# Performance work log

Hardware: AMD Instinct MI355X
Metric: run time of the kernel (lower is better)

## Reference

```python
import jax, jax.numpy as jnp
import numpy as np

N_NODES = 50000
IN_C, HID_C, OUT_C = 128, 128, 64
N_EDGES = 600000
DROPOUT_P = 0.5


def setup_inputs() -> dict:
    key = jax.random.key(0)
    k1, k2, k3, k4, k5, k6 = jax.random.split(key, 6)
    x = jax.random.normal(k1, (N_NODES, IN_C), dtype=jnp.float32)
    edge_index = jax.random.randint(k2, (2, N_EDGES), 0, N_NODES, dtype=jnp.int64)
    s1 = 1.0 / np.sqrt(IN_C)
    s2 = 1.0 / np.sqrt(HID_C)
    W1 = jax.random.uniform(k3, (IN_C, HID_C), jnp.float32, -s1, s1)
    b1 = jnp.zeros((HID_C,), jnp.float32)
    W2 = jax.random.uniform(k4, (HID_C, OUT_C), jnp.float32, -s2, s2)
    b2 = jnp.zeros((OUT_C,), jnp.float32)
    return {"x": x, "W1": W1, "b1": b1, "W2": W2, "b2": b2, "edge_index": edge_index}


def reference(x, W1, b1, W2, b2, edge_index):
    N = x.shape[0]
    self_loops = jnp.arange(N, dtype=edge_index.dtype)
    src = jnp.concatenate([edge_index[0], self_loops])  # [E+N]
    dst = jnp.concatenate([edge_index[1], self_loops])
    # symmetric GCN normalization with self-loops (gcn_norm)
    deg = jax.ops.segment_sum(jnp.ones(dst.shape, x.dtype), dst, num_segments=N)
    dinv = jnp.where(deg > 0, jax.lax.rsqrt(deg), 0.0)
    norm = dinv[src] * dinv[dst]  # [E+N]

    def conv(h, W, b):
        h = h @ W  # dense transform first (smaller message dim)
        msg = h[src] * norm[:, None]  # gather + scale, [E+N, C]
        return jax.ops.segment_sum(msg, dst, num_segments=N) + b

    h = jax.nn.relu(conv(x, W1, b1))
    # dropout p=0.5 with fixed key (training mode, deterministic reference)
    keep = jax.random.bernoulli(jax.random.key(42), 1.0 - DROPOUT_P, h.shape)
    h = jnp.where(keep, h / (1.0 - DROPOUT_P), 0.0)
    return conv(h, W2, b2)
```

## Files before the change

kernel.cpp:

```cpp
#include <hip/hip_runtime.h>


#define NN      50000
#define INC     128
#define HIDC    128
#define OUTC    64
#define NE      600000
#define NB      ((NN + 255) / 256)
#define CAP     64

typedef unsigned short bf16_t;
typedef short bf16x8 __attribute__((ext_vector_type(8)));
typedef float f32x4  __attribute__((ext_vector_type(4)));

__device__ __forceinline__ unsigned short f2bf(float f) {
  unsigned u = __float_as_uint(f);
  u += 0x7fffu + ((u >> 16) & 1u);
  return (unsigned short)(u >> 16);
}

__device__ __forceinline__ float dinv_of(int c) {
  return 1.0f / sqrtf((float)(c + 1));
}

__device__ __forceinline__ void tf_round(unsigned &x0, unsigned &x1, int r) {
  x0 += x1;
  x1 = (x1 << r) | (x1 >> (32 - r));
  x1 ^= x0;
}

__device__ __forceinline__ void threefry_0_42(unsigned &x0, unsigned &x1) {
  const unsigned ks0 = 0u, ks1 = 42u, ks2 = 0x1BD11BDAu ^ 42u;
  x0 += ks0; x1 += ks1;
  tf_round(x0,x1,13); tf_round(x0,x1,15); tf_round(x0,x1,26); tf_round(x0,x1, 6);
  x0 += ks1; x1 += ks2 + 1u;
  tf_round(x0,x1,17); tf_round(x0,x1,29); tf_round(x0,x1,16); tf_round(x0,x1,24);
  x0 += ks2; x1 += ks0 + 2u;
  tf_round(x0,x1,13); tf_round(x0,x1,15); tf_round(x0,x1,26); tf_round(x0,x1, 6);
  x0 += ks0; x1 += ks1 + 3u;
  tf_round(x0,x1,17); tf_round(x0,x1,29); tf_round(x0,x1,16); tf_round(x0,x1,24);
  x0 += ks1; x1 += ks2 + 4u;
  tf_round(x0,x1,13); tf_round(x0,x1,15); tf_round(x0,x1,26); tf_round(x0,x1, 6);
  x0 += ks2; x1 += ks0 + 5u;
}

__device__ __forceinline__ bool keep_bit(unsigned idx) {
  unsigned x0 = 0u, x1 = idx;
  threefry_0_42(x0, x1);
  return ((x0 ^ x1) & 0x80000000u) == 0u;
}

__global__ __launch_bounds__(256)
void prep0(const unsigned* __restrict__ ew, int* __restrict__ flag,
           int* __restrict__ cnt) {
  const int b = blockIdx.x, t = threadIdx.x;
  if (b < NB) {
    int idx = b * 256 + t;
    if (idx < NN) cnt[idx] = 0;
  } else {
    __shared__ unsigned acc[256];
    unsigned v = 0;
    for (int i = t; i < 2048; i += 256) v |= ew[2 * i + 1];
    acc[t] = v;
    __syncthreads();
    for (int s = 128; s > 0; s >>= 1) {
      if (t < s) acc[t] |= acc[t + s];
      __syncthreads();
    }
    if (t == 0) *flag = (acc[0] == 0u) ? 1 : 0;
  }
}

__global__ __launch_bounds__(256, 3)
void gemm1_bucket(const float* __restrict__ X, const float* __restrict__ W,
                  const void* __restrict__ ei, const int* __restrict__ flag,
                  int* __restrict__ cnt, int* __restrict__ ssrc,
                  bf16_t* __restrict__ Ab) {
  constexpr int C  = HIDC;
  constexpr int K  = 128;
  constexpr int KS = 136;
  constexpr int CT16 = C / 16;
  __shared__ bf16_t xs[64 * KS];
  __shared__ bf16_t wsT[C * KS];

  const int tid = threadIdx.x;
  const int rb  = blockIdx.x * 64;

  const int eb = blockIdx.x * 768;
  int es[3], ed[3];
  bool ev[3];
  const bool i64 = (*flag != 0);
#pragma unroll
  for (int j = 0; j < 3; j++) {
    int e = eb + j * 256 + tid;
    ev[j] = (e < NE);
    es[j] = 0; ed[j] = 0;
    if (ev[j]) {
      if (i64) {
        es[j] = (int)((const long long*)ei)[e];
        ed[j] = (int)((const long long*)ei)[NE + e];
      } else {
        es[j] = ((const int*)ei)[e];
        ed[j] = ((const int*)ei)[NE + e];
      }
    }
  }
  int slot[3];
#pragma unroll
  for (int j = 0; j < 3; j++)
    slot[j] = ev[j] ? atomicAdd(&cnt[ed[j]], 1) : CAP;

  for (int i = tid; i < C * (K / 8); i += 256) {
    int nn = i % C, kc = i / C;
    ushort4 lo, hi;
    lo.x = f2bf(W[(size_t)(kc * 8 + 0) * C + nn]);
    lo.y = f2bf(W[(size_t)(kc * 8 + 1) * C + nn]);
    lo.z = f2bf(W[(size_t)(kc * 8 + 2) * C + nn]);
    lo.w = f2bf(W[(size_t)(kc * 8 + 3) * C + nn]);
    hi.x = f2bf(W[(size_t)(kc * 8 + 4) * C + nn]);
    hi.y = f2bf(W[(size_t)(kc * 8 + 5) * C + nn]);
    hi.z = f2bf(W[(size_t)(kc * 8 + 6) * C + nn]);
    hi.w = f2bf(W[(size_t)(kc * 8 + 7) * C + nn]);
    *(ushort4*)&wsT[nn * KS + kc * 8]     = lo;
    *(ushort4*)&wsT[nn * KS + kc * 8 + 4] = hi;
  }
  for (int i = tid; i < 64 * (K / 4); i += 256) {
    int r = i >> 5, kq = i & 31;
    int row = rb + r;
    ushort4 o = make_ushort4(0, 0, 0, 0);
    if (row < NN) {
      float4 v = *(const float4*)(X + (size_t)row * K + kq * 4);
      o.x = f2bf(v.x); o.y = f2bf(v.y); o.z = f2bf(v.z); o.w = f2bf(v.w);
    }
    *(ushort4*)&xs[r * KS + kq * 4] = o;
  }

#pragma unroll
  for (int j = 0; j < 3; j++)
    if (ev[j] && slot[j] < CAP) ssrc[ed[j] * CAP + slot[j]] = es[j];

  __syncthreads();

  const int wv   = tid >> 6;
  const int lane = tid & 63;
  const int m    = lane & 15;
  const int q    = lane >> 4;

  f32x4 acc[CT16];
#pragma unroll
  for (int c = 0; c < CT16; c++) acc[c] = (f32x4){0.f, 0.f, 0.f, 0.f};

#pragma unroll
  for (int k0 = 0; k0 < K; k0 += 32) {
    bf16x8 a = *(bf16x8*)&xs[(wv * 16 + m) * KS + k0 + q * 8];
#pragma unroll
    for (int c = 0; c < CT16; c++) {
      bf16x8 b = *(bf16x8*)&wsT[(c * 16 + m) * KS + k0 + q * 8];
      acc[c] = __builtin_amdgcn_mfma_f32_16x16x32_bf16(a, b, acc[c], 0, 0, 0);
    }
  }

  const int rowq = rb + wv * 16 + q * 4;
#pragma unroll
  for (int r = 0; r < 4; r++) {
    int row = rowq + r;
    if (row < NN) {
#pragma unroll
      for (int c = 0; c < CT16; c++)
        Ab[(size_t)row * C + c * 16 + m] = f2bf(acc[c][r]);
    }
  }
}

template<int C, bool IN_BF16>
__global__ __launch_bounds__(256, 3)
void gemm_mfma(const void* __restrict__ Xv, const float* __restrict__ W,
               const int* __restrict__ cnt, bf16_t* __restrict__ Ab, int n) {
  constexpr int K  = 128;
  constexpr int KS = 136;
  constexpr int CT16 = C / 16;
  __shared__ bf16_t xs[64 * KS];
  __shared__ bf16_t wsT[C * KS];

  const int tid = threadIdx.x;
  const int rb  = blockIdx.x * 64;

  for (int i = tid; i < C * (K / 8); i += 256) {
    int nn = i % C, kc = i / C;
    ushort4 lo, hi;
    lo.x = f2bf(W[(size_t)(kc * 8 + 0) * C + nn]);
    lo.y = f2bf(W[(size_t)(kc * 8 + 1) * C + nn]);
    lo.z = f2bf(W[(size_t)(kc * 8 + 2) * C + nn]);
    lo.w = f2bf(W[(size_t)(kc * 8 + 3) * C + nn]);
    hi.x = f2bf(W[(size_t)(kc * 8 + 4) * C + nn]);
    hi.y = f2bf(W[(size_t)(kc * 8 + 5) * C + nn]);
    hi.z = f2bf(W[(size_t)(kc * 8 + 6) * C + nn]);
    hi.w = f2bf(W[(size_t)(kc * 8 + 7) * C + nn]);
    *(ushort4*)&wsT[nn * KS + kc * 8]     = lo;
    *(ushort4*)&wsT[nn * KS + kc * 8 + 4] = hi;
  }
  for (int i = tid; i < 64 * (K / 4); i += 256) {
    int r = i >> 5, kq = i & 31;
    int row = rb + r;
    ushort4 o = make_ushort4(0, 0, 0, 0);
    if (row < n) {
      if (IN_BF16) {
        o = *(const ushort4*)((const bf16_t*)Xv + (size_t)row * K + kq * 4);
      } else {
        float4 v = *(const float4*)((const float*)Xv + (size_t)row * K + kq * 4);
        o.x = f2bf(v.x); o.y = f2bf(v.y); o.z = f2bf(v.z); o.w = f2bf(v.w);
      }
    }
    *(ushort4*)&xs[r * KS + kq * 4] = o;
  }
  __syncthreads();

  const int wv   = tid >> 6;
  const int lane = tid & 63;
  const int m    = lane & 15;
  const int q    = lane >> 4;

  f32x4 acc[CT16];
#pragma unroll
  for (int c = 0; c < CT16; c++) acc[c] = (f32x4){0.f, 0.f, 0.f, 0.f};

#pragma unroll
  for (int k0 = 0; k0 < K; k0 += 32) {
    bf16x8 a = *(bf16x8*)&xs[(wv * 16 + m) * KS + k0 + q * 8];
#pragma unroll
    for (int c = 0; c < CT16; c++) {
      bf16x8 b = *(bf16x8*)&wsT[(c * 16 + m) * KS + k0 + q * 8];
      acc[c] = __builtin_amdgcn_mfma_f32_16x16x32_bf16(a, b, acc[c], 0, 0, 0);
    }
  }

  const int rowq = rb + wv * 16 + q * 4;
#pragma unroll
  for (int r = 0; r < 4; r++) {
    int row = rowq + r;
    if (row < n) {
      float dv = dinv_of(cnt[row]);
#pragma unroll
      for (int c = 0; c < CT16; c++)
        Ab[(size_t)row * C + c * 16 + m] = f2bf(acc[c][r] * dv);
    }
  }
}

__device__ __forceinline__ void acc_u2(float4 &a, uint2 v) {
  a.x += __uint_as_float(v.x << 16);
  a.y += __uint_as_float(v.x & 0xffff0000u);
  a.z += __uint_as_float(v.y << 16);
  a.w += __uint_as_float(v.y & 0xffff0000u);
}

__device__ __forceinline__ void acc_u2s(float4 &a, uint2 v, float dv) {
  a.x = fmaf(dv, __uint_as_float(v.x << 16),         a.x);
  a.y = fmaf(dv, __uint_as_float(v.x & 0xffff0000u), a.y);
  a.z = fmaf(dv, __uint_as_float(v.y << 16),         a.z);
  a.w = fmaf(dv, __uint_as_float(v.y & 0xffff0000u), a.w);
}

__device__ __forceinline__ float dinv_fast(int c) {
  return rsqrtf((float)(c + 1));
}

__global__ __launch_bounds__(256)
void agg1(const bf16_t* __restrict__ A1b, const int* __restrict__ cnt,
          const int* __restrict__ ssrc, const float* __restrict__ b1,
          bf16_t* __restrict__ Hb) {
  int node = (blockIdx.x * 256 + threadIdx.x) >> 5;
  int lane = threadIdx.x & 31;
  if (node >= NN) return;

  const uint2* A4 = (const uint2*)A1b;
  const int cn = cnt[node];
  const float dn = dinv_of(cn);
  float4 acc = make_float4(0.f, 0.f, 0.f, 0.f);
  acc_u2s(acc, A4[(size_t)node * 32 + lane], dn);
  int e = node * CAP;
  int end = e + min(cn, CAP);
  for (; e + 3 < end; e += 4) {
    int s0 = ssrc[e], s1 = ssrc[e+1], s2 = ssrc[e+2], s3 = ssrc[e+3];
    uint2 v0 = A4[(size_t)s0 * 32 + lane];
    uint2 v1 = A4[(size_t)s1 * 32 + lane];
    uint2 v2 = A4[(size_t)s2 * 32 + lane];
    uint2 v3 = A4[(size_t)s3 * 32 + lane];
    float q0 = dinv_fast(cnt[s0]);
    float q1 = dinv_fast(cnt[s1]);
    float q2 = dinv_fast(cnt[s2]);
    float q3 = dinv_fast(cnt[s3]);
    acc_u2s(acc, v0, q0); acc_u2s(acc, v1, q1);
    acc_u2s(acc, v2, q2); acc_u2s(acc, v3, q3);
  }
  for (; e < end; e++) {
    int s = ssrc[e];
    acc_u2s(acc, A4[(size_t)s * 32 + lane], dinv_fast(cnt[s]));
  }

  int col = lane * 4;
  float4 bb = *(const float4*)&b1[col];
  float h0 = fmaxf(acc.x * dn + bb.x, 0.f);
  float h1 = fmaxf(acc.y * dn + bb.y, 0.f);
  float h2 = fmaxf(acc.z * dn + bb.z, 0.f);
  float h3 = fmaxf(acc.w * dn + bb.w, 0.f);
  unsigned base = (unsigned)node * HIDC + (unsigned)col;
  ushort4 o;
  o.x = keep_bit(base)     ? f2bf(2.f * h0) : 0;
  o.y = keep_bit(base + 1) ? f2bf(2.f * h1) : 0;
  o.z = keep_bit(base + 2) ? f2bf(2.f * h2) : 0;
  o.w = keep_bit(base + 3) ? f2bf(2.f * h3) : 0;
  ((ushort4*)Hb)[(size_t)node * 32 + lane] = o;
}

__global__ __launch_bounds__(256)
void agg2(const bf16_t* __restrict__ A2b, const int* __restrict__ cnt,
          const int* __restrict__ ssrc, const float* __restrict__ b2,
          float* __restrict__ out) {
  int node = (blockIdx.x * 256 + threadIdx.x) >> 4;
  int lane = threadIdx.x & 15;
  if (node >= NN) return;

  const uint2* A4 = (const uint2*)A2b;
  const int cn = cnt[node];
  const float dn = dinv_of(cn);
  float4 acc = make_float4(0.f, 0.f, 0.f, 0.f);
  acc_u2(acc, A4[(size_t)node * 16 + lane]);
  int e = node * CAP;
  int end = e + min(cn, CAP);
  for (; e + 3 < end; e += 4) {
    int s0 = ssrc[e], s1 = ssrc[e+1], s2 = ssrc[e+2], s3 = ssrc[e+3];
    uint2 v0 = A4[(size_t)s0 * 16 + lane];
    uint2 v1 = A4[(size_t)s1 * 16 + lane];
    uint2 v2 = A4[(size_t)s2 * 16 + lane];
    uint2 v3 = A4[(size_t)s3 * 16 + lane];
    acc_u2(acc, v0); acc_u2(acc, v1); acc_u2(acc, v2); acc_u2(acc, v3);
  }
  for (; e < end; e++)
    acc_u2(acc, A4[(size_t)ssrc[e] * 16 + lane]);

  float4 bb = *(const float4*)&b2[lane * 4];
  ((float4*)out)[(size_t)node * 16 + lane] =
    make_float4(acc.x*dn + bb.x, acc.y*dn + bb.y, acc.z*dn + bb.z, acc.w*dn + bb.w);
}

extern "C" void kernel_launch(void* const* d_in, const int* in_sizes, int n_in,
                              void* d_out, int out_size, void* d_ws, size_t ws_size,
                              hipStream_t stream) {
  const float* x  = (const float*)d_in[0];
  const float* W1 = (const float*)d_in[1];
  const float* b1 = (const float*)d_in[2];
  const float* W2 = (const float*)d_in[3];
  const float* b2 = (const float*)d_in[4];
  const void*  ei = d_in[5];
  float* out = (float*)d_out;

  int*    flag = (int*)d_ws;
  int*    cnt  = flag + 64;
  int*    ssrc = cnt + 50048;
  bf16_t* A1b  = (bf16_t*)(ssrc + NN * CAP);
  bf16_t* Hb   = A1b + 6400000;
  bf16_t* A2b  = Hb + 6400000;

  prep0<<<NB + 1, 256, 0, stream>>>((const unsigned*)ei, flag, cnt);

  const int rtiles = (NN + 63) / 64;

  gemm1_bucket<<<rtiles, 256, 0, stream>>>(x, W1, ei, flag, cnt, ssrc, A1b);
  agg1<<<(NN * 32 + 255) / 256, 256, 0, stream>>>(A1b, cnt, ssrc, b1, Hb);

  gemm_mfma<OUTC, true><<<rtiles, 256, 0, stream>>>(Hb, W2, cnt, A2b, NN);
  agg2<<<(NN * 16 + 255) / 256, 256, 0, stream>>>(A2b, cnt, ssrc, b2, out);
}
```

Before: 185.9 us.

## Fuse layer-1 aggregation with layer-2 GEMM and narrow edge source indices

Merges the first aggregation (with ReLU, bias and dropout) into the second dense transform, so each block aggregates 64 nodes into shared memory and then runs MFMA on them directly. This removes the global hidden-activation buffer round trip and one kernel launch. Source indices in the bucket table are stored as 16-bit values to halve gather-index traffic, and the degree atomics in the first GEMM are deferred until after the shared-memory barrier. In exchange, each block serializes eight nodes per half-wave before the GEMM, which lowers gather parallelism per block.

```diff
diff --git a/kernel.cpp b/kernel.cpp
--- a/kernel.cpp
+++ b/kernel.cpp
@@ -21,6 +21,10 @@
 
 __device__ __forceinline__ float dinv_of(int c) {
   return 1.0f / sqrtf((float)(c + 1));
+}
+
+__device__ __forceinline__ float dinv_fast(int c) {
+  return rsqrtf((float)(c + 1));
 }
 
 __device__ __forceinline__ void tf_round(unsigned &x0, unsigned &x1, int r) {
@@ -74,7 +78,7 @@
 __global__ __launch_bounds__(256, 3)
 void gemm1_bucket(const float* __restrict__ X, const float* __restrict__ W,
                   const void* __restrict__ ei, const int* __restrict__ flag,
-                  int* __restrict__ cnt, int* __restrict__ ssrc,
+                  int* __restrict__ cnt, unsigned short* __restrict__ ssrc,
                   bf16_t* __restrict__ Ab) {
   constexpr int C  = HIDC;
   constexpr int K  = 128;
@@ -105,10 +109,6 @@
       }
     }
   }
-  int slot[3];
-#pragma unroll
-  for (int j = 0; j < 3; j++)
-    slot[j] = ev[j] ? atomicAdd(&cnt[ed[j]], 1) : CAP;
 
   for (int i = tid; i < C * (K / 8); i += 256) {
     int nn = i % C, kc = i / C;
@@ -135,11 +135,12 @@
     *(ushort4*)&xs[r * KS + kq * 4] = o;
   }
 
+  __syncthreads();
+
+  int slot[3];
 #pragma unroll
   for (int j = 0; j < 3; j++)
-    if (ev[j] && slot[j] < CAP) ssrc[ed[j] * CAP + slot[j]] = es[j];
-
-  __syncthreads();
+    slot[j] = ev[j] ? atomicAdd(&cnt[ed[j]], 1) : CAP;
 
   const int wv   = tid >> 6;
   const int lane = tid & 63;
@@ -170,81 +171,11 @@
         Ab[(size_t)row * C + c * 16 + m] = f2bf(acc[c][r]);
     }
   }
-}
-
-template<int C, bool IN_BF16>
-__global__ __launch_bounds__(256, 3)
-void gemm_mfma(const void* __restrict__ Xv, const float* __restrict__ W,
-               const int* __restrict__ cnt, bf16_t* __restrict__ Ab, int n) {
-  constexpr int K  = 128;
-  constexpr int KS = 136;
-  constexpr int CT16 = C / 16;
-  __shared__ bf16_t xs[64 * KS];
-  __shared__ bf16_t wsT[C * KS];
-
-  const int tid = threadIdx.x;
-  const int rb  = blockIdx.x * 64;
-
-  for (int i = tid; i < C * (K / 8); i += 256) {
-    int nn = i % C, kc = i / C;
-    ushort4 lo, hi;
-    lo.x = f2bf(W[(size_t)(kc * 8 + 0) * C + nn]);
-    lo.y = f2bf(W[(size_t)(kc * 8 + 1) * C + nn]);
-    lo.z = f2bf(W[(size_t)(kc * 8 + 2) * C + nn]);
-    lo.w = f2bf(W[(size_t)(kc * 8 + 3) * C + nn]);
-    hi.x = f2bf(W[(size_t)(kc * 8 + 4) * C + nn]);
-    hi.y = f2bf(W[(size_t)(kc * 8 + 5) * C + nn]);
-    hi.z = f2bf(W[(size_t)(kc * 8 + 6) * C + nn]);
-    hi.w = f2bf(W[(size_t)(kc * 8 + 7) * C + nn]);
-    *(ushort4*)&wsT[nn * KS + kc * 8]     = lo;
-    *(ushort4*)&wsT[nn * KS + kc * 8 + 4] = hi;
-  }
-  for (int i = tid; i < 64 * (K / 4); i += 256) {
-    int r = i >> 5, kq = i & 31;
-    int row = rb + r;
-    ushort4 o = make_ushort4(0, 0, 0, 0);
-    if (row < n) {
-      if (IN_BF16) {
-        o = *(const ushort4*)((const bf16_t*)Xv + (size_t)row * K + kq * 4);
-      } else {
-        float4 v = *(const float4*)((const float*)Xv + (size_t)row * K + kq * 4);
-        o.x = f2bf(v.x); o.y = f2bf(v.y); o.z = f2bf(v.z); o.w = f2bf(v.w);
-      }
-    }
-    *(ushort4*)&xs[r * KS + kq * 4] = o;
-  }
-  __syncthreads();
-
-  const int wv   = tid >> 6;
-  const int lane = tid & 63;
-  const int m    = lane & 15;
-  const int q    = lane >> 4;
-
-  f32x4 acc[CT16];
-#pragma unroll
-  for (int c = 0; c < CT16; c++) acc[c] = (f32x4){0.f, 0.f, 0.f, 0.f};
-
-#pragma unroll
-  for (int k0 = 0; k0 < K; k0 += 32) {
-    bf16x8 a = *(bf16x8*)&xs[(wv * 16 + m) * KS + k0 + q * 8];
-#pragma unroll
-    for (int c = 0; c < CT16; c++) {
-      bf16x8 b = *(bf16x8*)&wsT[(c * 16 + m) * KS + k0 + q * 8];
-      acc[c] = __builtin_amdgcn_mfma_f32_16x16x32_bf16(a, b, acc[c], 0, 0, 0);
-    }
-  }
-
-  const int rowq = rb + wv * 16 + q * 4;
-#pragma unroll
-  for (int r = 0; r < 4; r++) {
-    int row = rowq + r;
-    if (row < n) {
-      float dv = dinv_of(cnt[row]);
-#pragma unroll
-      for (int c = 0; c < CT16; c++)
-        Ab[(size_t)row * C + c * 16 + m] = f2bf(acc[c][r] * dv);
-    }
-  }
+
+#pragma unroll
+  for (int j = 0; j < 3; j++)
+    if (ev[j] && slot[j] < CAP)
+      ssrc[ed[j] * CAP + slot[j]] = (unsigned short)es[j];
 }
 
 __device__ __forceinline__ void acc_u2(float4 &a, uint2 v) {
@@ -261,62 +192,122 @@
   a.w = fmaf(dv, __uint_as_float(v.y & 0xffff0000u), a.w);
 }
 
-__device__ __forceinline__ float dinv_fast(int c) {
-  return rsqrtf((float)(c + 1));
-}
-
-__global__ __launch_bounds__(256)
-void agg1(const bf16_t* __restrict__ A1b, const int* __restrict__ cnt,
-          const int* __restrict__ ssrc, const float* __restrict__ b1,
-          bf16_t* __restrict__ Hb) {
-  int node = (blockIdx.x * 256 + threadIdx.x) >> 5;
-  int lane = threadIdx.x & 31;
-  if (node >= NN) return;
-
-  const uint2* A4 = (const uint2*)A1b;
-  const int cn = cnt[node];
-  const float dn = dinv_of(cn);
-  float4 acc = make_float4(0.f, 0.f, 0.f, 0.f);
-  acc_u2s(acc, A4[(size_t)node * 32 + lane], dn);
-  int e = node * CAP;
-  int end = e + min(cn, CAP);
-  for (; e + 3 < end; e += 4) {
-    int s0 = ssrc[e], s1 = ssrc[e+1], s2 = ssrc[e+2], s3 = ssrc[e+3];
-    uint2 v0 = A4[(size_t)s0 * 32 + lane];
-    uint2 v1 = A4[(size_t)s1 * 32 + lane];
-    uint2 v2 = A4[(size_t)s2 * 32 + lane];
-    uint2 v3 = A4[(size_t)s3 * 32 + lane];
-    float q0 = dinv_fast(cnt[s0]);
-    float q1 = dinv_fast(cnt[s1]);
-    float q2 = dinv_fast(cnt[s2]);
-    float q3 = dinv_fast(cnt[s3]);
-    acc_u2s(acc, v0, q0); acc_u2s(acc, v1, q1);
-    acc_u2s(acc, v2, q2); acc_u2s(acc, v3, q3);
-  }
-  for (; e < end; e++) {
-    int s = ssrc[e];
-    acc_u2s(acc, A4[(size_t)s * 32 + lane], dinv_fast(cnt[s]));
-  }
-
-  int col = lane * 4;
-  float4 bb = *(const float4*)&b1[col];
-  float h0 = fmaxf(acc.x * dn + bb.x, 0.f);
-  float h1 = fmaxf(acc.y * dn + bb.y, 0.f);
-  float h2 = fmaxf(acc.z * dn + bb.z, 0.f);
-  float h3 = fmaxf(acc.w * dn + bb.w, 0.f);
-  unsigned base = (unsigned)node * HIDC + (unsigned)col;
-  ushort4 o;
-  o.x = keep_bit(base)     ? f2bf(2.f * h0) : 0;
-  o.y = keep_bit(base + 1) ? f2bf(2.f * h1) : 0;
-  o.z = keep_bit(base + 2) ? f2bf(2.f * h2) : 0;
-  o.w = keep_bit(base + 3) ? f2bf(2.f * h3) : 0;
-  ((ushort4*)Hb)[(size_t)node * 32 + lane] = o;
+__global__ __launch_bounds__(256, 4)
+void agg1_gemm2(const bf16_t* __restrict__ A1b, const int* __restrict__ cnt,
+                const unsigned short* __restrict__ ssrc,
+                const float* __restrict__ b1, const float* __restrict__ W2,
+                bf16_t* __restrict__ A2b) {
+  constexpr int C  = OUTC;
+  constexpr int K  = HIDC;
+  constexpr int KS = 136;
+  constexpr int CT16 = C / 16;
+  __shared__ bf16_t xs[64 * KS];
+  __shared__ bf16_t wsT[C * KS];
+
+  const int tid = threadIdx.x;
+  const int rb  = blockIdx.x * 64;
+
+  for (int i = tid; i < C * (K / 8); i += 256) {
+    int nn = i % C, kc = i / C;
+    ushort4 lo, hi;
+    lo.x = f2bf(W2[(size_t)(kc * 8 + 0) * C + nn]);
+    lo.y = f2bf(W2[(size_t)(kc * 8 + 1) * C + nn]);
+    lo.z = f2bf(W2[(size_t)(kc * 8 + 2) * C + nn]);
+    lo.w = f2bf(W2[(size_t)(kc * 8 + 3) * C + nn]);
+    hi.x = f2bf(W2[(size_t)(kc * 8 + 4) * C + nn]);
+    hi.y = f2bf(W2[(size_t)(kc * 8 + 5) * C + nn]);
+    hi.z = f2bf(W2[(size_t)(kc * 8 + 6) * C + nn]);
+    hi.w = f2bf(W2[(size_t)(kc * 8 + 7) * C + nn]);
+    *(ushort4*)&wsT[nn * KS + kc * 8]     = lo;
+    *(ushort4*)&wsT[nn * KS + kc * 8 + 4] = hi;
+  }
+
+  {
+    const int hw   = tid >> 5;
+    const int lane = tid & 31;
+    const int col  = lane * 4;
+    const float4 bb = *(const float4*)&b1[col];
+    const uint2* A4 = (const uint2*)A1b;
+
+    for (int i = 0; i < 8; i++) {
+      const int r    = hw * 8 + i;
+      const int node = rb + r;
+      ushort4 o = make_ushort4(0, 0, 0, 0);
+      if (node < NN) {
+        const int cn = cnt[node];
+        const float dn = dinv_of(cn);
+        float4 acc = make_float4(0.f, 0.f, 0.f, 0.f);
+        acc_u2s(acc, A4[(size_t)node * 32 + lane], dn);
+        int e = node * CAP;
+        int end = e + min(cn, CAP);
+        for (; e + 3 < end; e += 4) {
+          int s0 = ssrc[e], s1 = ssrc[e+1], s2 = ssrc[e+2], s3 = ssrc[e+3];
+          uint2 v0 = A4[(size_t)s0 * 32 + lane];
+          uint2 v1 = A4[(size_t)s1 * 32 + lane];
+          uint2 v2 = A4[(size_t)s2 * 32 + lane];
+          uint2 v3 = A4[(size_t)s3 * 32 + lane];
+          float q0 = dinv_fast(cnt[s0]);
+          float q1 = dinv_fast(cnt[s1]);
+          float q2 = dinv_fast(cnt[s2]);
+          float q3 = dinv_fast(cnt[s3]);
+          acc_u2s(acc, v0, q0); acc_u2s(acc, v1, q1);
+          acc_u2s(acc, v2, q2); acc_u2s(acc, v3, q3);
+        }
+        for (; e < end; e++) {
+          int s = ssrc[e];
+          acc_u2s(acc, A4[(size_t)s * 32 + lane], dinv_fast(cnt[s]));
+        }
+        float h0 = fmaxf(acc.x * dn + bb.x, 0.f);
+        float h1 = fmaxf(acc.y * dn + bb.y, 0.f);
+        float h2 = fmaxf(acc.z * dn + bb.z, 0.f);
+        float h3 = fmaxf(acc.w * dn + bb.w, 0.f);
+        unsigned base = (unsigned)node * HIDC + (unsigned)col;
+        o.x = keep_bit(base)     ? f2bf(2.f * h0) : 0;
+        o.y = keep_bit(base + 1) ? f2bf(2.f * h1) : 0;
+        o.z = keep_bit(base + 2) ? f2bf(2.f * h2) : 0;
+        o.w = keep_bit(base + 3) ? f2bf(2.f * h3) : 0;
+      }
+      *(ushort4*)&xs[r * KS + col] = o;
+    }
+  }
+  __syncthreads();
+
+  const int wv   = tid >> 6;
+  const int lane = tid & 63;
+  const int m    = lane & 15;
+  const int q    = lane >> 4;
+
+  f32x4 acc[CT16];
+#pragma unroll
+  for (int c = 0; c < CT16; c++) acc[c] = (f32x4){0.f, 0.f, 0.f, 0.f};
+
+#pragma unroll
+  for (int k0 = 0; k0 < K; k0 += 32) {
+    bf16x8 a = *(bf16x8*)&xs[(wv * 16 + m) * KS + k0 + q * 8];
+#pragma unroll
+    for (int c = 0; c < CT16; c++) {
+      bf16x8 b = *(bf16x8*)&wsT[(c * 16 + m) * KS + k0 + q * 8];
+      acc[c] = __builtin_amdgcn_mfma_f32_16x16x32_bf16(a, b, acc[c], 0, 0, 0);
+    }
+  }
+
+  const int rowq = rb + wv * 16 + q * 4;
+#pragma unroll
+  for (int r = 0; r < 4; r++) {
+    int row = rowq + r;
+    if (row < NN) {
+      float dv = dinv_of(cnt[row]);
+#pragma unroll
+      for (int c = 0; c < CT16; c++)
+        A2b[(size_t)row * C + c * 16 + m] = f2bf(acc[c][r] * dv);
+    }
+  }
 }
 
 __global__ __launch_bounds__(256)
 void agg2(const bf16_t* __restrict__ A2b, const int* __restrict__ cnt,
-          const int* __restrict__ ssrc, const float* __restrict__ b2,
-          float* __restrict__ out) {
+          const unsigned short* __restrict__ ssrc,
+          const float* __restrict__ b2, float* __restrict__ out) {
   int node = (blockIdx.x * 256 + threadIdx.x) >> 4;
   int lane = threadIdx.x & 15;
   if (node >= NN) return;
@@ -355,20 +346,19 @@
   const void*  ei = d_in[5];
   float* out = (float*)d_out;
 
-  int*    flag = (int*)d_ws;
-  int*    cnt  = flag + 64;
-  int*    ssrc = cnt + 50048;
-  bf16_t* A1b  = (bf16_t*)(ssrc + NN * CAP);
-  bf16_t* Hb   = A1b + 6400000;
-  bf16_t* A2b  = Hb + 6400000;
+  int*            flag = (int*)d_ws;
+  int*            cnt  = flag + 64;
+  unsigned short* ssrc = (unsigned short*)(cnt + 50048);
+  bf16_t*         A1b  = (bf16_t*)(ssrc + NN * CAP);
+  bf16_t*         A2b  = A1b + 6400000;
 
   prep0<<<NB + 1, 256, 0, stream>>>((const unsigned*)ei, flag, cnt);
 
   const int rtiles = (NN + 63) / 64;
 
   gemm1_bucket<<<rtiles, 256, 0, stream>>>(x, W1, ei, flag, cnt, ssrc, A1b);
-  agg1<<<(NN * 32 + 255) / 256, 256, 0, stream>>>(A1b, cnt, ssrc, b1, Hb);
-
-  gemm_mfma<OUTC, true><<<rtiles, 256, 0, stream>>>(Hb, W2, cnt, A2b, NN);
+
+  agg1_gemm2<<<rtiles, 256, 0, stream>>>(A1b, cnt, ssrc, b1, W2, A2b);
+
   agg2<<<(NN * 16 + 255) / 256, 256, 0, stream>>>(A2b, cnt, ssrc, b2, out);
 }
```

Result: slower. 200.1 us (+7.6%).
